# Optimization experiments

Measured on AMD Instinct MI355X. Metric: run time of the kernel, lower is better.

The kernel has to match this reference:

```python
import jax, jax.numpy as jnp
import numpy as np

N = 100000
E = 1600000
IN_F = 128
OUT_F = 64
ALPHA = 0.2  # leaky relu slope
EPS = 1e-16


def setup_inputs() -> dict:
    key = jax.random.key(0)
    k1, k2, k3, k4 = jax.random.split(key, 4)
    x = jax.random.normal(k1, (N, IN_F), dtype=jnp.float32)
    edge_index = jax.random.randint(k2, (2, E), 0, N, dtype=jnp.int64)
    # xavier_uniform with gain=1.414
    gain = 1.414
    limW = gain * np.sqrt(6.0 / (IN_F + OUT_F))
    W = jax.random.uniform(k3, (IN_F, OUT_F), minval=-limW, maxval=limW, dtype=jnp.float32)
    lima = gain * np.sqrt(6.0 / (2 * OUT_F + 1))
    a = jax.random.uniform(k4, (2 * OUT_F, 1), minval=-lima, maxval=lima, dtype=jnp.float32)
    return {"x": x, "edge_index": edge_index, "W": W, "a": a}


def reference(x, edge_index, W, a):
    src = edge_index[0]
    tgt = edge_index[1]
    Wh = x @ W  # (N, out)
    # e = leakyrelu([Wh[src] || Wh[tgt]] @ a) ; split a to avoid materializing concat
    a_src = a[:OUT_F, 0]
    a_tgt = a[OUT_F:, 0]
    score_src = Wh @ a_src  # (N,)
    score_tgt = Wh @ a_tgt  # (N,)
    e = jax.nn.leaky_relu(score_src[src] + score_tgt[tgt], ALPHA)  # (E,)
    # segment softmax over edges grouped by target node
    e_max = jax.ops.segment_max(e, tgt, num_segments=N)  # -inf for empty segments, never gathered
    e_exp = jnp.exp(e - e_max[tgt])
    e_sum = jax.ops.segment_sum(e_exp, tgt, num_segments=N)
    alpha = e_exp / (e_sum[tgt] + EPS)  # (E,)
    # dropout is identity in eval mode
    v_weighted = Wh[src] * alpha[:, None]  # (E, out)
    h_prime = jax.ops.segment_sum(v_weighted, tgt, num_segments=N)  # (N, out)
    return jax.nn.elu(h_prime)  # concat=True branch
```

## Files before the change

### kernel.cpp

```cpp
#include <hip/hip_runtime.h>

#define N_NODES 100000
#define N_EDGES 1600000
#define IN_FEAT 128
#define OUT_FEAT 64
#define LRELU_SLOPE 0.2f
#define EPS_DENOM 1e-16f

#define SB_SHIFT 8
#define SB_NODES 256
#define NSB 391
#define N_SUB 8
#define SUBA_CAP 704
#define STAGE_CAP 4608
#define SWIN (STAGE_CAP + SB_NODES)
#define CH 4096
#define SCAT_BLOCKS ((N_EDGES + CH - 1) / CH)
#define GEMM_BLOCKS ((N_NODES + 63) / 64)

typedef __attribute__((ext_vector_type(8))) short bf16x8;
typedef __attribute__((ext_vector_type(4))) float f32x4;

__device__ __forceinline__ unsigned int enc_f(float x) {
    unsigned int u = __float_as_uint(x);
    return (u & 0x80000000u) ? ~u : (u | 0x80000000u);
}
__device__ __forceinline__ float dec_f(unsigned int u) {
    u = (u & 0x80000000u) ? (u ^ 0x80000000u) : ~u;
    return __uint_as_float(u);
}
#define ENC_NEG_INF 0x007FFFFFu

__device__ __forceinline__ unsigned short f2bf(float f) {
    unsigned int u = __float_as_uint(f);
    u = (u + 0x7FFFu + ((u >> 16) & 1u)) >> 16;
    return (unsigned short)u;
}

__global__ __launch_bounds__(256) void init_prep_kernel(
    const float* __restrict__ W, int* __restrict__ cursorA,
    unsigned short* __restrict__ WTb)
{
    const int i = blockIdx.x * 256 + threadIdx.x;
    if (i < NSB * N_SUB) cursorA[i] = i * SUBA_CAP;
    if (i < OUT_FEAT * IN_FEAT) {
        const int n = i >> 7, k = i & 127;
        WTb[i] = f2bf(W[k * OUT_FEAT + n]);
    }
}

struct GemmS {
    unsigned short xs[64][136];
    float ssp[4][64];
    float stp[4][64];
};
struct ScatS {
    int staged[CH];
    int hcnt[NSB];
    int gbase[NSB];
    int lcnt[NSB];
    int lbase[NSB];
    int pfx[256];
};

__global__ __launch_bounds__(256) void gemm_scatter_kernel(
    const float* __restrict__ x, const unsigned short* __restrict__ WTb,
    const float* __restrict__ a, const int* __restrict__ ei,
    int* __restrict__ cursorA, int* __restrict__ bucketsA,
    unsigned short* __restrict__ WhB,
    float* __restrict__ s_src, float* __restrict__ s_tgt)
{
    __shared__ __align__(16) char smem[sizeof(ScatS) > sizeof(GemmS) ? sizeof(ScatS)
                                                                     : sizeof(GemmS)];
    const int tid = threadIdx.x;

    if (blockIdx.x < SCAT_BLOCKS) {
        ScatS& S = *(ScatS*)smem;
        const int base = blockIdx.x * CH;
        const int sub = blockIdx.x & (N_SUB - 1);
        for (int j = tid; j < NSB; j += 256) S.hcnt[j] = 0;
        __syncthreads();
        int tloc[CH / 256], sloc[CH / 256];
        #pragma unroll
        for (int k = 0; k < CH / 256; ++k) {
            const int i = base + k * 256 + tid;
            tloc[k] = (i < N_EDGES) ? ei[N_EDGES + i] : -1;
            sloc[k] = (i < N_EDGES) ? ei[i] : 0;
            if (tloc[k] >= 0) atomicAdd(&S.hcnt[tloc[k] >> SB_SHIFT], 1);
        }
        __syncthreads();
        int carry = 0;
        for (int c0 = 0; c0 < NSB; c0 += 256) {
            const int idx = c0 + tid;
            const int v = (idx < NSB) ? S.hcnt[idx] : 0;
            S.pfx[tid] = v;
            __syncthreads();
            for (int off = 1; off < 256; off <<= 1) {
                const int add = (tid >= off) ? S.pfx[tid - off] : 0;
                __syncthreads();
                S.pfx[tid] += add;
                __syncthreads();
            }
            if (idx < NSB) S.lbase[idx] = carry + S.pfx[tid] - v;
            carry += S.pfx[255];
            __syncthreads();
        }
        for (int j = tid; j < NSB; j += 256) {
            S.lcnt[j] = 0;
            const int c = S.hcnt[j];
            S.gbase[j] = c ? atomicAdd(&cursorA[j * N_SUB + sub], c) : 0;
        }
        __syncthreads();
        #pragma unroll
        for (int k = 0; k < CH / 256; ++k) {
            if (tloc[k] >= 0) {
                const int sb = tloc[k] >> SB_SHIFT;
                const int r = atomicAdd(&S.lcnt[sb], 1);
                S.staged[S.lbase[sb] + r] = sloc[k] | ((tloc[k] & (SB_NODES - 1)) << 17);
            }
        }
        __syncthreads();
        const int grp = tid >> 4, gl = tid & 15;
        for (int sb = grp; sb < NSB; sb += 16) {
            const int c = S.hcnt[sb];
            const int lb = S.lbase[sb];
            const int gb = S.gbase[sb];
            for (int k = gl; k < c; k += 16) bucketsA[gb + k] = S.staged[lb + k];
        }
        return;
    }

    GemmS& G = *(GemmS*)smem;
    const int wid = tid >> 6, lane = tid & 63;
    const int r0 = (blockIdx.x - SCAT_BLOCKS) * 64;

    #pragma unroll
    for (int it = 0; it < 8; ++it) {
        const int idx4 = it * 256 + tid;
        const int row = idx4 >> 5;
        const int col = (idx4 & 31) * 4;
        float4 v = make_float4(0.f, 0.f, 0.f, 0.f);
        if (r0 + row < N_NODES) v = *(const float4*)(x + (size_t)(r0 + row) * IN_FEAT + col);
        const unsigned int p0 = (unsigned int)f2bf(v.x) | ((unsigned int)f2bf(v.y) << 16);
        const unsigned int p1 = (unsigned int)f2bf(v.z) | ((unsigned int)f2bf(v.w) << 16);
        *(uint2*)&G.xs[row][col] = make_uint2(p0, p1);
    }
    __syncthreads();

    const int cgrp = lane >> 4;
    const int cl = lane & 15;
    const int col = wid * 16 + cl;
    f32x4 acc0 = {0.f,0.f,0.f,0.f}, acc1 = acc0, acc2 = acc0, acc3 = acc0;
    #pragma unroll
    for (int kb = 0; kb < IN_FEAT; kb += 32) {
        const bf16x8 bfrag = *(const bf16x8*)(WTb + col * IN_FEAT + kb + cgrp * 8);
        const bf16x8 a0 = *(const bf16x8*)&G.xs[ 0 + cl][kb + cgrp * 8];
        const bf16x8 a1 = *(const bf16x8*)&G.xs[16 + cl][kb + cgrp * 8];
        const bf16x8 a2 = *(const bf16x8*)&G.xs[32 + cl][kb + cgrp * 8];
        const bf16x8 a3 = *(const bf16x8*)&G.xs[48 + cl][kb + cgrp * 8];
        acc0 = __builtin_amdgcn_mfma_f32_16x16x32_bf16(a0, bfrag, acc0, 0, 0, 0);
        acc1 = __builtin_amdgcn_mfma_f32_16x16x32_bf16(a1, bfrag, acc1, 0, 0, 0);
        acc2 = __builtin_amdgcn_mfma_f32_16x16x32_bf16(a2, bfrag, acc2, 0, 0, 0);
        acc3 = __builtin_amdgcn_mfma_f32_16x16x32_bf16(a3, bfrag, acc3, 0, 0, 0);
    }

    const float a_s = a[col], a_t = a[OUT_FEAT + col];
    #pragma unroll
    for (int mt = 0; mt < 4; ++mt) {
        const f32x4 av = (mt == 0) ? acc0 : (mt == 1) ? acc1 : (mt == 2) ? acc2 : acc3;
        #pragma unroll
        for (int r = 0; r < 4; ++r) {
            const int lrow = mt * 16 + cgrp * 4 + r;
            const float v = av[r];
            const int grow = r0 + lrow;
            if (grow < N_NODES) WhB[(size_t)grow * OUT_FEAT + col] = f2bf(v);
            float ss = v * a_s;
            float st = v * a_t;
            #pragma unroll
            for (int off = 1; off < 16; off <<= 1) {
                ss += __shfl_xor(ss, off, 64);
                st += __shfl_xor(st, off, 64);
            }
            if (cl == 0) { G.ssp[wid][lrow] = ss; G.stp[wid][lrow] = st; }
        }
    }
    __syncthreads();
    if (tid < 64 && r0 + tid < N_NODES) {
        s_src[r0 + tid] = (G.ssp[0][tid] + G.ssp[1][tid]) + (G.ssp[2][tid] + G.ssp[3][tid]);
        s_tgt[r0 + tid] = (G.stp[0][tid] + G.stp[1][tid]) + (G.stp[2][tid] + G.stp[3][tid]);
    }
}

__global__ __launch_bounds__(512) void sort_sb_kernel(
    const int* __restrict__ cursorA, const int* __restrict__ bucketsA,
    const float* __restrict__ s_src, const float* __restrict__ s_tgt,
    int2* __restrict__ sorted_se, unsigned int* __restrict__ segA)
{
    __shared__ int2 stage[STAGE_CAP];
    __shared__ float stgt[SB_NODES];
    __shared__ int cnt[SB_NODES];
    __shared__ int pfx[SB_NODES];
    __shared__ int cur[SB_NODES];
    __shared__ unsigned int m_enc[SB_NODES];
    __shared__ int c_ofs[N_SUB + 1];
    const int b = blockIdx.x;
    const int tid = threadIdx.x;

    if (tid < SB_NODES) {
        cnt[tid] = 0;
        m_enc[tid] = ENC_NEG_INF;
        const int node = b * SB_NODES + tid;
        stgt[tid] = (node < N_NODES) ? s_tgt[node] : 0.0f;
    }
    if (tid == 0) {
        int o = 0;
        #pragma unroll
        for (int s = 0; s < N_SUB; ++s) {
            c_ofs[s] = o;
            o += cursorA[b * N_SUB + s] - (b * N_SUB + s) * SUBA_CAP;
        }
        c_ofs[N_SUB] = o;
    }
    __syncthreads();
    const int tot = c_ofs[N_SUB];
    #pragma unroll
    for (int s = 0; s < N_SUB; ++s) {
        const int o = c_ofs[s];
        const int c = c_ofs[s + 1] - o;
        const int* src = bucketsA + (size_t)(b * N_SUB + s) * SUBA_CAP;
        for (int k = tid; k < c; k += 512) {
            const int pk = src[k];
            const int tl = (pk >> 17) & (SB_NODES - 1);
            float v = s_src[pk & 0x1FFFF] + stgt[tl];
            v = (v >= 0.0f) ? v : LRELU_SLOPE * v;
            stage[o + k] = make_int2(pk, __float_as_int(v));
            atomicAdd(&cnt[tl], 1);
            atomicMax(&m_enc[tl], enc_f(v));
        }
    }
    __syncthreads();
    if (tid < SB_NODES) pfx[tid] = (cnt[tid] + 1) & ~1;
    __syncthreads();
    for (int off = 1; off < SB_NODES; off <<= 1) {
        const int add = (tid < SB_NODES && tid >= off) ? pfx[tid - off] : 0;
        __syncthreads();
        if (tid < SB_NODES) pfx[tid] += add;
        __syncthreads();
    }
    if (tid < SB_NODES) {
        const int ex = pfx[tid] - ((cnt[tid] + 1) & ~1);
        cur[tid] = ex;
        const int node = b * SB_NODES + tid;
        if (node < N_NODES)
            segA[node] = ((unsigned int)(b * SWIN + ex) << 10) | (unsigned int)cnt[tid];
    }
    __syncthreads();
    for (int i = tid; i < tot; i += 512) {
        const int2 pk = stage[i];
        const int tl = (pk.x >> 17) & (SB_NODES - 1);
        const int pos = atomicAdd(&cur[tl], 1);
        const float w = __expf(__int_as_float(pk.y) - dec_f(m_enc[tl]));
        sorted_se[(size_t)b * SWIN + pos] = make_int2(pk.x & 0x1FFFF, __float_as_int(w));
    }
}

__global__ __launch_bounds__(256) void node_aggr_kernel(
    const unsigned int* __restrict__ segA, const int2* __restrict__ sorted_se,
    const unsigned short* __restrict__ WhB, float* __restrict__ out)
{
    const int gtid = blockIdx.x * 256 + threadIdx.x;
    const int node = gtid >> 4;
    const int gl = threadIdx.x & 15;
    const unsigned int sg = segA[node];
    const int beg = (int)(sg >> 10);
    const int end = beg + (int)(sg & 1023u);

    const char* whb = (const char*)WhB;
    const unsigned int foff = (unsigned int)gl << 3;
    float a0 = 0.f, a1 = 0.f, a2 = 0.f, a3 = 0.f, sum = 0.f;
    int i = beg;
    for (; i + 4 <= end; i += 4) {
        const int4 q0 = *(const int4*)&sorted_se[i];
        const int4 q1 = *(const int4*)&sorted_se[i + 2];
        const unsigned int s0 = (unsigned int)q0.x & 0x1FFFFu;
        const unsigned int s1 = (unsigned int)q0.z & 0x1FFFFu;
        const unsigned int s2 = (unsigned int)q1.x & 0x1FFFFu;
        const unsigned int s3 = (unsigned int)q1.z & 0x1FFFFu;
        const uint2 g0 = *(const uint2*)(whb + ((s0 << 7) + foff));
        const uint2 g1 = *(const uint2*)(whb + ((s1 << 7) + foff));
        const uint2 g2 = *(const uint2*)(whb + ((s2 << 7) + foff));
        const uint2 g3 = *(const uint2*)(whb + ((s3 << 7) + foff));
        const float w0 = __int_as_float(q0.y), w1 = __int_as_float(q0.w);
        const float w2 = __int_as_float(q1.y), w3 = __int_as_float(q1.w);
        a0 += w0 * __uint_as_float(g0.x << 16) + w1 * __uint_as_float(g1.x << 16)
            + w2 * __uint_as_float(g2.x << 16) + w3 * __uint_as_float(g3.x << 16);
        a1 += w0 * __uint_as_float(g0.x & 0xFFFF0000u) + w1 * __uint_as_float(g1.x & 0xFFFF0000u)
            + w2 * __uint_as_float(g2.x & 0xFFFF0000u) + w3 * __uint_as_float(g3.x & 0xFFFF0000u);
        a2 += w0 * __uint_as_float(g0.y << 16) + w1 * __uint_as_float(g1.y << 16)
            + w2 * __uint_as_float(g2.y << 16) + w3 * __uint_as_float(g3.y << 16);
        a3 += w0 * __uint_as_float(g0.y & 0xFFFF0000u) + w1 * __uint_as_float(g1.y & 0xFFFF0000u)
            + w2 * __uint_as_float(g2.y & 0xFFFF0000u) + w3 * __uint_as_float(g3.y & 0xFFFF0000u);
        sum += (w0 + w1) + (w2 + w3);
    }
    if (i + 2 <= end) {
        const int4 q0 = *(const int4*)&sorted_se[i];
        const unsigned int s0 = (unsigned int)q0.x & 0x1FFFFu;
        const unsigned int s1 = (unsigned int)q0.z & 0x1FFFFu;
        const uint2 g0 = *(const uint2*)(whb + ((s0 << 7) + foff));
        const uint2 g1 = *(const uint2*)(whb + ((s1 << 7) + foff));
        const float w0 = __int_as_float(q0.y), w1 = __int_as_float(q0.w);
        a0 += w0 * __uint_as_float(g0.x << 16) + w1 * __uint_as_float(g1.x << 16);
        a1 += w0 * __uint_as_float(g0.x & 0xFFFF0000u) + w1 * __uint_as_float(g1.x & 0xFFFF0000u);
        a2 += w0 * __uint_as_float(g0.y << 16) + w1 * __uint_as_float(g1.y << 16);
        a3 += w0 * __uint_as_float(g0.y & 0xFFFF0000u) + w1 * __uint_as_float(g1.y & 0xFFFF0000u);
        sum += w0 + w1;
        i += 2;
    }
    if (i < end) {
        const int2 pk = sorted_se[i];
        const unsigned int s0 = (unsigned int)pk.x & 0x1FFFFu;
        const uint2 g0 = *(const uint2*)(whb + ((s0 << 7) + foff));
        const float w0 = __int_as_float(pk.y);
        a0 += w0 * __uint_as_float(g0.x << 16);
        a1 += w0 * __uint_as_float(g0.x & 0xFFFF0000u);
        a2 += w0 * __uint_as_float(g0.y << 16);
        a3 += w0 * __uint_as_float(g0.y & 0xFFFF0000u);
        sum += w0;
    }

    const float inv = 1.0f / (sum + EPS_DENOM);
    float4 o;
    o.x = a0 * inv; o.y = a1 * inv; o.z = a2 * inv; o.w = a3 * inv;
    o.x = (o.x > 0.f) ? o.x : expm1f(o.x);
    o.y = (o.y > 0.f) ? o.y : expm1f(o.y);
    o.z = (o.z > 0.f) ? o.z : expm1f(o.z);
    o.w = (o.w > 0.f) ? o.w : expm1f(o.w);
    *(float4*)(out + (size_t)node * OUT_FEAT + (gl << 2)) = o;
}

extern "C" void kernel_launch(void* const* d_in, const int* in_sizes, int n_in,
                              void* d_out, int out_size, void* d_ws, size_t ws_size,
                              hipStream_t stream) {
    const float* x  = (const float*)d_in[0];
    const int*   ei = (const int*)d_in[1];
    const float* W  = (const float*)d_in[2];
    const float* a  = (const float*)d_in[3];
    float* out = (float*)d_out;

    char* p = (char*)d_ws;
    unsigned short* WhB = (unsigned short*)p; p += (size_t)N_NODES * OUT_FEAT * 2;
    unsigned short* WTb = (unsigned short*)p; p += (size_t)OUT_FEAT * IN_FEAT * 2;
    float* s_src    = (float*)p;  p += (size_t)N_NODES * 4;
    float* s_tgt    = (float*)p;  p += (size_t)N_NODES * 4;
    unsigned int* segA = (unsigned int*)p; p += (size_t)N_NODES * 4;
    int*   cursorA  = (int*)p;    p += (size_t)NSB * N_SUB * 4;
    p = (char*)(((size_t)p + 15) & ~(size_t)15);
    int*   bucketsA = (int*)p;    p += (size_t)NSB * N_SUB * SUBA_CAP * 4;
    int2*  sorted_se = (int2*)p;  p += (size_t)NSB * SWIN * 8;

    init_prep_kernel<<<32, 256, 0, stream>>>(W, cursorA, WTb);
    gemm_scatter_kernel<<<SCAT_BLOCKS + GEMM_BLOCKS, 256, 0, stream>>>(
        x, WTb, a, ei, cursorA, bucketsA, WhB, s_src, s_tgt);
    sort_sb_kernel<<<NSB, 512, 0, stream>>>(cursorA, bucketsA, s_src, s_tgt, sorted_se, segA);
    node_aggr_kernel<<<(N_NODES * 16) / 256, 256, 0, stream>>>(segA, sorted_se, WhB, out);
}
```

Measured before the change: 101.7 us.

## Fuse per-superblock sort and node aggregation into one kernel via LDS

Merges the sort kernel and the node aggregation kernel so each 256-node superblock keeps its sorted (src, weight) pairs in shared memory and aggregates them directly, instead of writing them and a segment table to global memory and reading them back in a second launch. This removes a global round trip and a kernel launch. In exchange, LDS use per block roughly doubles (a second 36 KB array), and only 391 blocks of 512 threads do the gather work with 8 nodes per 16-lane group, so there is less parallelism and latency hiding for the WhB gathers.

```diff
diff --git a/kernel.cpp b/kernel.cpp
--- a/kernel.cpp
+++ b/kernel.cpp
@@ -13,7 +13,6 @@
 #define N_SUB 8
 #define SUBA_CAP 704
 #define STAGE_CAP 4608
-#define SWIN (STAGE_CAP + SB_NODES)
 #define CH 4096
 #define SCAT_BLOCKS ((N_EDGES + CH - 1) / CH)
 #define GEMM_BLOCKS ((N_NODES + 63) / 64)
@@ -191,12 +190,13 @@
     }
 }
 
-__global__ __launch_bounds__(512) void sort_sb_kernel(
+__global__ __launch_bounds__(512) void sort_aggr_kernel(
     const int* __restrict__ cursorA, const int* __restrict__ bucketsA,
     const float* __restrict__ s_src, const float* __restrict__ s_tgt,
-    int2* __restrict__ sorted_se, unsigned int* __restrict__ segA)
+    const unsigned short* __restrict__ WhB, float* __restrict__ out)
 {
     __shared__ int2 stage[STAGE_CAP];
+    __shared__ int2 sorted[STAGE_CAP];
     __shared__ float stgt[SB_NODES];
     __shared__ int cnt[SB_NODES];
     __shared__ int pfx[SB_NODES];
@@ -239,7 +239,7 @@
         }
     }
     __syncthreads();
-    if (tid < SB_NODES) pfx[tid] = (cnt[tid] + 1) & ~1;
+    if (tid < SB_NODES) pfx[tid] = cnt[tid];
     __syncthreads();
     for (int off = 1; off < SB_NODES; off <<= 1) {
         const int add = (tid < SB_NODES && tid >= off) ? pfx[tid - off] : 0;
@@ -248,11 +248,9 @@
         __syncthreads();
     }
     if (tid < SB_NODES) {
-        const int ex = pfx[tid] - ((cnt[tid] + 1) & ~1);
+        const int ex = pfx[tid] - cnt[tid];
         cur[tid] = ex;
-        const int node = b * SB_NODES + tid;
-        if (node < N_NODES)
-            segA[node] = ((unsigned int)(b * SWIN + ex) << 10) | (unsigned int)cnt[tid];
+        pfx[tid] = ex;
     }
     __syncthreads();
     for (int i = tid; i < tot; i += 512) {
@@ -260,82 +258,60 @@
         const int tl = (pk.x >> 17) & (SB_NODES - 1);
         const int pos = atomicAdd(&cur[tl], 1);
         const float w = __expf(__int_as_float(pk.y) - dec_f(m_enc[tl]));
-        sorted_se[(size_t)b * SWIN + pos] = make_int2(pk.x & 0x1FFFF, __float_as_int(w));
-    }
-}
-
-__global__ __launch_bounds__(256) void node_aggr_kernel(
-    const unsigned int* __restrict__ segA, const int2* __restrict__ sorted_se,
-    const unsigned short* __restrict__ WhB, float* __restrict__ out)
-{
-    const int gtid = blockIdx.x * 256 + threadIdx.x;
-    const int node = gtid >> 4;
-    const int gl = threadIdx.x & 15;
-    const unsigned int sg = segA[node];
-    const int beg = (int)(sg >> 10);
-    const int end = beg + (int)(sg & 1023u);
-
+        sorted[pos] = make_int2(pk.x & 0x1FFFF, __float_as_int(w));
+    }
+    __syncthreads();
+
+    const int grp = tid >> 4, gl = tid & 15;
     const char* whb = (const char*)WhB;
     const unsigned int foff = (unsigned int)gl << 3;
-    float a0 = 0.f, a1 = 0.f, a2 = 0.f, a3 = 0.f, sum = 0.f;
-    int i = beg;
-    for (; i + 4 <= end; i += 4) {
-        const int4 q0 = *(const int4*)&sorted_se[i];
-        const int4 q1 = *(const int4*)&sorted_se[i + 2];
-        const unsigned int s0 = (unsigned int)q0.x & 0x1FFFFu;
-        const unsigned int s1 = (unsigned int)q0.z & 0x1FFFFu;
-        const unsigned int s2 = (unsigned int)q1.x & 0x1FFFFu;
-        const unsigned int s3 = (unsigned int)q1.z & 0x1FFFFu;
-        const uint2 g0 = *(const uint2*)(whb + ((s0 << 7) + foff));
-        const uint2 g1 = *(const uint2*)(whb + ((s1 << 7) + foff));
-        const uint2 g2 = *(const uint2*)(whb + ((s2 << 7) + foff));
-        const uint2 g3 = *(const uint2*)(whb + ((s3 << 7) + foff));
-        const float w0 = __int_as_float(q0.y), w1 = __int_as_float(q0.w);
-        const float w2 = __int_as_float(q1.y), w3 = __int_as_float(q1.w);
-        a0 += w0 * __uint_as_float(g0.x << 16) + w1 * __uint_as_float(g1.x << 16)
-            + w2 * __uint_as_float(g2.x << 16) + w3 * __uint_as_float(g3.x << 16);
-        a1 += w0 * __uint_as_float(g0.x & 0xFFFF0000u) + w1 * __uint_as_float(g1.x & 0xFFFF0000u)
-            + w2 * __uint_as_float(g2.x & 0xFFFF0000u) + w3 * __uint_as_float(g3.x & 0xFFFF0000u);
-        a2 += w0 * __uint_as_float(g0.y << 16) + w1 * __uint_as_float(g1.y << 16)
-            + w2 * __uint_as_float(g2.y << 16) + w3 * __uint_as_float(g3.y << 16);
-        a3 += w0 * __uint_as_float(g0.y & 0xFFFF0000u) + w1 * __uint_as_float(g1.y & 0xFFFF0000u)
-            + w2 * __uint_as_float(g2.y & 0xFFFF0000u) + w3 * __uint_as_float(g3.y & 0xFFFF0000u);
-        sum += (w0 + w1) + (w2 + w3);
-    }
-    if (i + 2 <= end) {
-        const int4 q0 = *(const int4*)&sorted_se[i];
-        const unsigned int s0 = (unsigned int)q0.x & 0x1FFFFu;
-        const unsigned int s1 = (unsigned int)q0.z & 0x1FFFFu;
-        const uint2 g0 = *(const uint2*)(whb + ((s0 << 7) + foff));
-        const uint2 g1 = *(const uint2*)(whb + ((s1 << 7) + foff));
-        const float w0 = __int_as_float(q0.y), w1 = __int_as_float(q0.w);
-        a0 += w0 * __uint_as_float(g0.x << 16) + w1 * __uint_as_float(g1.x << 16);
-        a1 += w0 * __uint_as_float(g0.x & 0xFFFF0000u) + w1 * __uint_as_float(g1.x & 0xFFFF0000u);
-        a2 += w0 * __uint_as_float(g0.y << 16) + w1 * __uint_as_float(g1.y << 16);
-        a3 += w0 * __uint_as_float(g0.y & 0xFFFF0000u) + w1 * __uint_as_float(g1.y & 0xFFFF0000u);
-        sum += w0 + w1;
-        i += 2;
-    }
-    if (i < end) {
-        const int2 pk = sorted_se[i];
-        const unsigned int s0 = (unsigned int)pk.x & 0x1FFFFu;
-        const uint2 g0 = *(const uint2*)(whb + ((s0 << 7) + foff));
-        const float w0 = __int_as_float(pk.y);
-        a0 += w0 * __uint_as_float(g0.x << 16);
-        a1 += w0 * __uint_as_float(g0.x & 0xFFFF0000u);
-        a2 += w0 * __uint_as_float(g0.y << 16);
-        a3 += w0 * __uint_as_float(g0.y & 0xFFFF0000u);
-        sum += w0;
-    }
-
-    const float inv = 1.0f / (sum + EPS_DENOM);
-    float4 o;
-    o.x = a0 * inv; o.y = a1 * inv; o.z = a2 * inv; o.w = a3 * inv;
-    o.x = (o.x > 0.f) ? o.x : expm1f(o.x);
-    o.y = (o.y > 0.f) ? o.y : expm1f(o.y);
-    o.z = (o.z > 0.f) ? o.z : expm1f(o.z);
-    o.w = (o.w > 0.f) ? o.w : expm1f(o.w);
-    *(float4*)(out + (size_t)node * OUT_FEAT + (gl << 2)) = o;
+    #pragma unroll
+    for (int n = 0; n < 8; ++n) {
+        const int nl = grp * 8 + n;
+        const int node = b * SB_NODES + nl;
+        if (node >= N_NODES) continue;
+        const int beg = pfx[nl];
+        const int end = beg + cnt[nl];
+        float a0 = 0.f, a1 = 0.f, a2 = 0.f, a3 = 0.f, sum = 0.f;
+        int i = beg;
+        for (; i + 4 <= end; i += 4) {
+            const int2 p0 = sorted[i],     p1 = sorted[i + 1];
+            const int2 p2 = sorted[i + 2], p3 = sorted[i + 3];
+            const uint2 g0 = *(const uint2*)(whb + (((unsigned int)p0.x << 7) + foff));
+            const uint2 g1 = *(const uint2*)(whb + (((unsigned int)p1.x << 7) + foff));
+            const uint2 g2 = *(const uint2*)(whb + (((unsigned int)p2.x << 7) + foff));
+            const uint2 g3 = *(const uint2*)(whb + (((unsigned int)p3.x << 7) + foff));
+            const float w0 = __int_as_float(p0.y), w1 = __int_as_float(p1.y);
+            const float w2 = __int_as_float(p2.y), w3 = __int_as_float(p3.y);
+            a0 += w0 * __uint_as_float(g0.x << 16) + w1 * __uint_as_float(g1.x << 16)
+                + w2 * __uint_as_float(g2.x << 16) + w3 * __uint_as_float(g3.x << 16);
+            a1 += w0 * __uint_as_float(g0.x & 0xFFFF0000u) + w1 * __uint_as_float(g1.x & 0xFFFF0000u)
+                + w2 * __uint_as_float(g2.x & 0xFFFF0000u) + w3 * __uint_as_float(g3.x & 0xFFFF0000u);
+            a2 += w0 * __uint_as_float(g0.y << 16) + w1 * __uint_as_float(g1.y << 16)
+                + w2 * __uint_as_float(g2.y << 16) + w3 * __uint_as_float(g3.y << 16);
+            a3 += w0 * __uint_as_float(g0.y & 0xFFFF0000u) + w1 * __uint_as_float(g1.y & 0xFFFF0000u)
+                + w2 * __uint_as_float(g2.y & 0xFFFF0000u) + w3 * __uint_as_float(g3.y & 0xFFFF0000u);
+            sum += (w0 + w1) + (w2 + w3);
+        }
+        for (; i < end; ++i) {
+            const int2 pk = sorted[i];
+            const uint2 g0 = *(const uint2*)(whb + (((unsigned int)pk.x << 7) + foff));
+            const float w0 = __int_as_float(pk.y);
+            a0 += w0 * __uint_as_float(g0.x << 16);
+            a1 += w0 * __uint_as_float(g0.x & 0xFFFF0000u);
+            a2 += w0 * __uint_as_float(g0.y << 16);
+            a3 += w0 * __uint_as_float(g0.y & 0xFFFF0000u);
+            sum += w0;
+        }
+        const float inv = 1.0f / (sum + EPS_DENOM);
+        float4 o;
+        o.x = a0 * inv; o.y = a1 * inv; o.z = a2 * inv; o.w = a3 * inv;
+        o.x = (o.x > 0.f) ? o.x : expm1f(o.x);
+        o.y = (o.y > 0.f) ? o.y : expm1f(o.y);
+        o.z = (o.z > 0.f) ? o.z : expm1f(o.z);
+        o.w = (o.w > 0.f) ? o.w : expm1f(o.w);
+        *(float4*)(out + (size_t)node * OUT_FEAT + (gl << 2)) = o;
+    }
 }
 
 extern "C" void kernel_launch(void* const* d_in, const int* in_sizes, int n_in,
@@ -352,15 +328,12 @@
     unsigned short* WTb = (unsigned short*)p; p += (size_t)OUT_FEAT * IN_FEAT * 2;
     float* s_src    = (float*)p;  p += (size_t)N_NODES * 4;
     float* s_tgt    = (float*)p;  p += (size_t)N_NODES * 4;
-    unsigned int* segA = (unsigned int*)p; p += (size_t)N_NODES * 4;
     int*   cursorA  = (int*)p;    p += (size_t)NSB * N_SUB * 4;
     p = (char*)(((size_t)p + 15) & ~(size_t)15);
     int*   bucketsA = (int*)p;    p += (size_t)NSB * N_SUB * SUBA_CAP * 4;
-    int2*  sorted_se = (int2*)p;  p += (size_t)NSB * SWIN * 8;
 
     init_prep_kernel<<<32, 256, 0, stream>>>(W, cursorA, WTb);
     gemm_scatter_kernel<<<SCAT_BLOCKS + GEMM_BLOCKS, 256, 0, stream>>>(
         x, WTb, a, ei, cursorA, bucketsA, WhB, s_src, s_tgt);
-    sort_sb_kernel<<<NSB, 512, 0, stream>>>(cursorA, bucketsA, s_src, s_tgt, sorted_se, segA);
-    node_aggr_kernel<<<(N_NODES * 16) / 256, 256, 0, stream>>>(segA, sorted_se, WhB, out);
-}
+    sort_aggr_kernel<<<NSB, 512, 0, stream>>>(cursorA, bucketsA, s_src, s_tgt, WhB, out);
+}
```

Result: faster. 96.55 us (-5.0%).
